# Kernel tuning notes

Hardware: AMD Instinct MI355X
Metric: run time of the kernel (lower is better)

The kernel has to match this reference:

```python
import jax, jax.numpy as jnp
import numpy as np

DECAY = 0.99
BETA = 0.25
EPS_NORM = 1e-12  # matches F.normalize eps


def _l2_normalize(x):
    n = jnp.linalg.norm(x, axis=-1, keepdims=True)
    return x / jnp.maximum(n, EPS_NORM)


def setup_inputs() -> dict:
    key = jax.random.key(0)
    ks = jax.random.split(key, 8)
    B, C, H, W = 16, 256, 64, 64
    D, K = 16, 4096  # codebook_dim, n_embed
    z = jax.random.normal(ks[0], (B, C, H, W), dtype=jnp.float32)
    # 1x1 convs == per-pixel linear layers
    w_down = jax.random.normal(ks[1], (D, C), dtype=jnp.float32) / np.sqrt(C).astype(np.float32)
    b_down = jnp.zeros((D,), dtype=jnp.float32)
    w_up = jax.random.normal(ks[2], (C, D), dtype=jnp.float32) / np.sqrt(D).astype(np.float32)
    b_up = jnp.zeros((C,), dtype=jnp.float32)
    embedding = jax.random.uniform(ks[3], (K, D), minval=-1.0 / K, maxval=1.0 / K, dtype=jnp.float32)
    cluster_size = jax.random.uniform(ks[4], (K,), minval=0.5, maxval=2.0, dtype=jnp.float32)
    embed_avg = jax.random.normal(ks[5], (K, D), dtype=jnp.float32) * 0.01
    return {"z": z, "w_down": w_down, "b_down": b_down, "w_up": w_up,
            "b_up": b_up, "embedding": embedding,
            "cluster_size": cluster_size, "embed_avg": embed_avg}


def reference(z, w_down, b_down, w_up, b_up, embedding, cluster_size, embed_avg):
    B, C, H, W = z.shape
    K, D = embedding.shape

    # proj_down: 1x1 conv -> per-token linear
    z_low = jnp.einsum('bchw,dc->bdhw', z, w_down) + b_down[None, :, None, None]
    z_flat = z_low.transpose(0, 2, 3, 1).reshape(-1, D)          # [N, D]
    z_norm = _l2_normalize(z_flat)
    e_norm = _l2_normalize(embedding)                             # [K, D]

    # squared L2 distances (argmin identical to cdist argmin)
    d2 = (jnp.sum(z_norm * z_norm, -1, keepdims=True)
          - 2.0 * z_norm @ e_norm.T
          + jnp.sum(e_norm * e_norm, -1)[None, :])               # [N, K]
    indices = jnp.argmin(d2, axis=-1)                             # [N]
    z_q_flat = e_norm[indices]                                    # [N, D]

    # EMA buffer update (training path); scatter-accumulate via segment_sum
    ones = jnp.ones(indices.shape, dtype=jnp.float32)
    batch_cluster_size = jax.ops.segment_sum(ones, indices, num_segments=K)
    batch_embed_sum = jax.ops.segment_sum(z_norm, indices, num_segments=K)
    new_cluster_size = cluster_size * DECAY + (1.0 - DECAY) * batch_cluster_size
    new_embed_avg = embed_avg * DECAY + (1.0 - DECAY) * batch_embed_sum
    n = new_cluster_size.sum()
    cs = (new_cluster_size + 1e-5) / (n + K * 1e-5) * n
    new_embedding = new_embed_avg / cs[:, None]

    commitment_loss = BETA * jnp.mean((z_norm - jax.lax.stop_gradient(z_q_flat)) ** 2)

    # straight-through estimator
    z_q_low_flat = z_norm + jax.lax.stop_gradient(z_q_flat - z_norm)
    z_q_low = z_q_low_flat.reshape(B, H, W, D).transpose(0, 3, 1, 2)
    z_q = jnp.einsum('bdhw,cd->bchw', z_q_low, w_up) + b_up[None, :, None, None]

    indices_2d = indices.reshape(B, H, W)

    # metrics / entropy loss (usage == bincount(indices))
    usage_prob = batch_cluster_size / (batch_cluster_size.sum() + 1e-8)
    entropy = -jnp.sum(usage_prob * jnp.log(usage_prob + 1e-8))
    entropy_loss = jnp.log(jnp.float32(K)) - entropy

    return (z_q, commitment_loss, indices_2d, entropy_loss,
            new_embedding, new_cluster_size, new_embed_avg)
```

## Files before the change

kernel.cpp:

```cpp
#include <hip/hip_runtime.h>
#include <math.h>

#define NTOK 65536
#define CDIM 256
#define DDIM 16
#define KCOD 4096
#define HWSZ 4096

#define DELTA 0.04f
#define KSPLIT2 8
#define KTPS (KCOD / 32 / KSPLIT2)

typedef short short8 __attribute__((ext_vector_type(8)));
typedef float f32x16 __attribute__((ext_vector_type(16)));

#define WS_ENORM 0
#define WS_ENN   (WS_ENORM + KCOD*DDIM)
#define WS_WDT   (WS_ENN + KCOD)
#define WS_EBF   (WS_WDT + CDIM*DDIM)
#define WS_ZN    (WS_EBF + KCOD*8)
#define WS_ZNBF  (WS_ZN + NTOK*DDIM)
#define WS_M1    (WS_ZNBF + NTOK*8)
#define WS_BCS   (WS_M1 + NTOK)
#define WS_BES   (WS_BCS + KCOD)
#define WS_SCAL  (WS_BES + KCOD*DDIM)
#define WS_PACK  (WS_SCAL + 8)

#define OFS_ZQ   0
#define OFS_LOSS 16777216
#define OFS_IDX  16777217
#define OFS_ENT  16842753
#define OFS_NE   16842754
#define OFS_NCS  16908290
#define OFS_NEA  16912386

__device__ inline unsigned f2bf2(float lo, float hi) {
  unsigned a = __float_as_uint(lo), b = __float_as_uint(hi);
  a = (a + 0x7FFFu + ((a >> 16) & 1u)) >> 16;
  b = (b + 0x7FFFu + ((b >> 16) & 1u)) >> 16;
  return a | (b << 16);
}
__device__ inline unsigned flipf(float f) {
  unsigned u = __float_as_uint(f);
  return (u & 0x80000000u) ? ~u : (u | 0x80000000u);
}
__device__ inline float unflipf(unsigned k) {
  unsigned u = (k & 0x80000000u) ? (k ^ 0x80000000u) : ~k;
  return __uint_as_float(u);
}

__global__ __launch_bounds__(256) void knorm_kernel(const float* __restrict__ emb,
                                                    const float* __restrict__ w_down,
                                                    float* __restrict__ ws) {
  int k = blockIdx.x * 256 + threadIdx.x;
  const float4* src = (const float4*)emb + (size_t)k * 4;
  float4 t0 = src[0], t1 = src[1], t2 = src[2], t3 = src[3];
  float e[16] = {t0.x,t0.y,t0.z,t0.w, t1.x,t1.y,t1.z,t1.w,
                 t2.x,t2.y,t2.z,t2.w, t3.x,t3.y,t3.z,t3.w};
  float ss = 0.f;
  #pragma unroll
  for (int d = 0; d < 16; ++d) ss += e[d] * e[d];
  float dn = fmaxf(sqrtf(ss), 1e-12f);
  #pragma unroll
  for (int d = 0; d < 16; ++d) e[d] = e[d] / dn;
  float s2 = 0.f;
  #pragma unroll
  for (int d = 0; d < 16; ++d) s2 += e[d] * e[d];
  float4* dst = (float4*)(ws + WS_ENORM) + (size_t)k * 4;
  dst[0] = make_float4(e[0],e[1],e[2],e[3]);
  dst[1] = make_float4(e[4],e[5],e[6],e[7]);
  dst[2] = make_float4(e[8],e[9],e[10],e[11]);
  dst[3] = make_float4(e[12],e[13],e[14],e[15]);
  ws[WS_ENN + k] = s2;
  ws[WS_WDT + k] = w_down[(k & 15) * 256 + (k >> 4)];
  uint4 p0 = make_uint4(f2bf2(e[0],e[1]),  f2bf2(e[2],e[3]),
                        f2bf2(e[4],e[5]),  f2bf2(e[6],e[7]));
  uint4 p1 = make_uint4(f2bf2(e[8],e[9]),  f2bf2(e[10],e[11]),
                        f2bf2(e[12],e[13]),f2bf2(e[14],e[15]));
  uint4* eb = (uint4*)(ws + WS_EBF) + (size_t)k * 2;
  eb[0] = p0; eb[1] = p1;
}

__global__ __launch_bounds__(256) void kdown_kernel(const float* __restrict__ z,
                                                    const float* __restrict__ wdt,
                                                    const float* __restrict__ b_down,
                                                    float* __restrict__ znp,
                                                    unsigned* __restrict__ znbf) {
  const int tid = threadIdx.x;
  const int n = blockIdx.x * 256 + tid;
  const int b = n >> 12;
  const int hw = n & 4095;
  const float* zp = z + (size_t)b * (CDIM * HWSZ) + hw;

  float acc[16];
  #pragma unroll
  for (int d = 0; d < 16; ++d) acc[d] = 0.f;

  #pragma unroll 16
  for (int c = 0; c < CDIM; ++c) {
    float zv = zp[(size_t)c * HWSZ];
    const float4* wr = (const float4*)(wdt + c * 16);
    float4 w0 = wr[0], w1 = wr[1], w2 = wr[2], w3 = wr[3];
    acc[0]  = fmaf(zv, w0.x, acc[0]);  acc[1]  = fmaf(zv, w0.y, acc[1]);
    acc[2]  = fmaf(zv, w0.z, acc[2]);  acc[3]  = fmaf(zv, w0.w, acc[3]);
    acc[4]  = fmaf(zv, w1.x, acc[4]);  acc[5]  = fmaf(zv, w1.y, acc[5]);
    acc[6]  = fmaf(zv, w1.z, acc[6]);  acc[7]  = fmaf(zv, w1.w, acc[7]);
    acc[8]  = fmaf(zv, w2.x, acc[8]);  acc[9]  = fmaf(zv, w2.y, acc[9]);
    acc[10] = fmaf(zv, w2.z, acc[10]); acc[11] = fmaf(zv, w2.w, acc[11]);
    acc[12] = fmaf(zv, w3.x, acc[12]); acc[13] = fmaf(zv, w3.y, acc[13]);
    acc[14] = fmaf(zv, w3.z, acc[14]); acc[15] = fmaf(zv, w3.w, acc[15]);
  }

  #pragma unroll
  for (int d = 0; d < 16; ++d) acc[d] = acc[d] + b_down[d];
  float ss = 0.f;
  #pragma unroll
  for (int d = 0; d < 16; ++d) ss += acc[d] * acc[d];
  float dn = fmaxf(sqrtf(ss), 1e-12f);
  #pragma unroll
  for (int d = 0; d < 16; ++d) acc[d] = acc[d] / dn;

  float4* op = (float4*)znp + (size_t)n * 4;
  op[0] = make_float4(acc[0],acc[1],acc[2],acc[3]);
  op[1] = make_float4(acc[4],acc[5],acc[6],acc[7]);
  op[2] = make_float4(acc[8],acc[9],acc[10],acc[11]);
  op[3] = make_float4(acc[12],acc[13],acc[14],acc[15]);

  uint4 p0 = make_uint4(f2bf2(acc[0],acc[1]),  f2bf2(acc[2],acc[3]),
                        f2bf2(acc[4],acc[5]),  f2bf2(acc[6],acc[7]));
  uint4 p1 = make_uint4(f2bf2(acc[8],acc[9]),  f2bf2(acc[10],acc[11]),
                        f2bf2(acc[12],acc[13]),f2bf2(acc[14],acc[15]));
  uint4* zb = (uint4*)znbf + (size_t)n * 2;
  zb[0] = p0; zb[1] = p1;
}

__global__ __launch_bounds__(256) void kmin_kernel(const unsigned* __restrict__ znbf,
                                                   const unsigned* __restrict__ ebf,
                                                   unsigned* __restrict__ m1u) {
  const int lane = threadIdx.x & 63;
  const int wv = threadIdx.x >> 6;
  const int tokbase = (blockIdx.x * 4 + wv) * 32;
  const int kt0 = blockIdx.y * KTPS;
  const int hi = lane >> 5;
  const int ln = lane & 31;

  const short8* za = (const short8*)znbf;
  const short8* eb = (const short8*)ebf;
  short8 afrag = za[(size_t)(tokbase + ln) * 2 + hi];

  float m[16];
  #pragma unroll
  for (int r = 0; r < 16; ++r) m[r] = -3.4e38f;

  #pragma unroll 4
  for (int kt = 0; kt < KTPS; ++kt) {
    short8 bfrag = eb[(size_t)((kt0 + kt) * 32 + ln) * 2 + hi];
    f32x16 acc;
    #pragma unroll
    for (int r = 0; r < 16; ++r) acc[r] = 0.f;
    acc = __builtin_amdgcn_mfma_f32_32x32x16_bf16(afrag, bfrag, acc, 0, 0, 0);
    #pragma unroll
    for (int r = 0; r < 16; ++r) m[r] = fmaxf(m[r], acc[r]);
  }

  #pragma unroll
  for (int r = 0; r < 16; ++r) {
    float v = m[r];
    v = fmaxf(v, __shfl_xor(v, 16, 32));
    v = fmaxf(v, __shfl_xor(v, 8, 32));
    v = fmaxf(v, __shfl_xor(v, 4, 32));
    v = fmaxf(v, __shfl_xor(v, 2, 32));
    v = fmaxf(v, __shfl_xor(v, 1, 32));
    m[r] = v;
  }
  if (ln == 0) {
    #pragma unroll
    for (int r = 0; r < 16; ++r) {
      int row = (r & 3) + 8 * (r >> 2) + 4 * hi;
      atomicMax(m1u + tokbase + row, flipf(m[r]));
    }
  }
}

__global__ __launch_bounds__(256) void kcand_kernel(const unsigned* __restrict__ znbf,
                                                    const unsigned* __restrict__ ebf,
                                                    const unsigned* __restrict__ m1u,
                                                    const float* __restrict__ enorm,
                                                    const float* __restrict__ ennp,
                                                    const float* __restrict__ znp,
                                                    unsigned long long* __restrict__ packp) {
  const int lane = threadIdx.x & 63;
  const int wv = threadIdx.x >> 6;
  const int tokbase = (blockIdx.x * 4 + wv) * 32;
  const int kt0 = blockIdx.y * KTPS;
  const int hi = lane >> 5;
  const int ln = lane & 31;

  const short8* za = (const short8*)znbf;
  const short8* eb = (const short8*)ebf;
  short8 afrag = za[(size_t)(tokbase + ln) * 2 + hi];

  float thr[16];
  #pragma unroll
  for (int r = 0; r < 16; ++r) {
    int row = (r & 3) + 8 * (r >> 2) + 4 * hi;
    thr[r] = unflipf(m1u[tokbase + row]) - DELTA;
  }

  for (int kt = 0; kt < KTPS; ++kt) {
    short8 bfrag = eb[(size_t)((kt0 + kt) * 32 + ln) * 2 + hi];
    f32x16 acc;
    #pragma unroll
    for (int r = 0; r < 16; ++r) acc[r] = 0.f;
    acc = __builtin_amdgcn_mfma_f32_32x32x16_bf16(afrag, bfrag, acc, 0, 0, 0);

    unsigned flags = 0u;
    #pragma unroll
    for (int r = 0; r < 16; ++r) flags |= (acc[r] >= thr[r]) ? (1u << r) : 0u;

    if (flags) {
      #pragma unroll
      for (int r = 0; r < 16; ++r) {
        if (flags & (1u << r)) {
          int row = (r & 3) + 8 * (r >> 2) + 4 * hi;
          int token = tokbase + row;
          int code = (kt0 + kt) * 32 + ln;
          const float4* znr4 = (const float4*)znp + (size_t)token * 4;
          const float4* er4  = (const float4*)enorm + (size_t)code * 4;
          float4 za0 = znr4[0], za1 = znr4[1], za2 = znr4[2], za3 = znr4[3];
          float4 eb0 = er4[0],  eb1 = er4[1],  eb2 = er4[2],  eb3 = er4[3];
          float dsc = ennp[code];
          dsc = fmaf(-2.f * za0.x, eb0.x, dsc); dsc = fmaf(-2.f * za0.y, eb0.y, dsc);
          dsc = fmaf(-2.f * za0.z, eb0.z, dsc); dsc = fmaf(-2.f * za0.w, eb0.w, dsc);
          dsc = fmaf(-2.f * za1.x, eb1.x, dsc); dsc = fmaf(-2.f * za1.y, eb1.y, dsc);
          dsc = fmaf(-2.f * za1.z, eb1.z, dsc); dsc = fmaf(-2.f * za1.w, eb1.w, dsc);
          dsc = fmaf(-2.f * za2.x, eb2.x, dsc); dsc = fmaf(-2.f * za2.y, eb2.y, dsc);
          dsc = fmaf(-2.f * za2.z, eb2.z, dsc); dsc = fmaf(-2.f * za2.w, eb2.w, dsc);
          dsc = fmaf(-2.f * za3.x, eb3.x, dsc); dsc = fmaf(-2.f * za3.y, eb3.y, dsc);
          dsc = fmaf(-2.f * za3.z, eb3.z, dsc); dsc = fmaf(-2.f * za3.w, eb3.w, dsc);
          unsigned u = __float_as_uint(dsc);
          u = (u & 0x80000000u) ? ~u : (u | 0x80000000u);
          unsigned long long key =
              ((unsigned long long)u << 32) | (unsigned)code;
          atomicMin(packp + token, key);
        }
      }
    }
  }
}

__global__ __launch_bounds__(256) void kfinal_kernel(const float* __restrict__ w_up,
                                                     const float* __restrict__ b_up,
                                                     const float* __restrict__ enorm,
                                                     const float* __restrict__ znp,
                                                     const unsigned long long* __restrict__ packp,
                                                     float* __restrict__ wsacc,
                                                     float* __restrict__ out) {
  const int tid = threadIdx.x;
  const int n = blockIdx.x * 256 + tid;
  const int bidx = (int)(unsigned)(packp[n] & 0xFFFFFFFFull);

  float zn[16];
  {
    const float4* zp = (const float4*)znp + (size_t)n * 4;
    float4 a0 = zp[0], a1 = zp[1], a2 = zp[2], a3 = zp[3];
    zn[0]=a0.x; zn[1]=a0.y; zn[2]=a0.z; zn[3]=a0.w;
    zn[4]=a1.x; zn[5]=a1.y; zn[6]=a1.z; zn[7]=a1.w;
    zn[8]=a2.x; zn[9]=a2.y; zn[10]=a2.z; zn[11]=a2.w;
    zn[12]=a3.x; zn[13]=a3.y; zn[14]=a3.z; zn[15]=a3.w;
  }
  float zq[16];
  {
    const float4* ebp = (const float4*)enorm + (size_t)bidx * 4;
    float4 q0 = ebp[0], q1 = ebp[1], q2 = ebp[2], q3 = ebp[3];
    zq[0]=q0.x; zq[1]=q0.y; zq[2]=q0.z; zq[3]=q0.w;
    zq[4]=q1.x; zq[5]=q1.y; zq[6]=q1.z; zq[7]=q1.w;
    zq[8]=q2.x; zq[9]=q2.y; zq[10]=q2.z; zq[11]=q2.w;
    zq[12]=q3.x; zq[13]=q3.y; zq[14]=q3.z; zq[15]=q3.w;
  }

  out[OFS_IDX + n] = (float)bidx;

  float ls = 0.f;
  #pragma unroll
  for (int d = 0; d < 16; ++d) { float df = zn[d] - zq[d]; ls = fmaf(df, df, ls); }

  atomicAdd(wsacc + bidx, 1.0f);
  #pragma unroll
  for (int d = 0; d < 16; ++d)
    atomicAdd(wsacc + KCOD + (size_t)bidx * 16 + d, zn[d]);

  #pragma unroll
  for (int off = 32; off > 0; off >>= 1) ls += __shfl_down(ls, off, 64);
  if ((tid & 63) == 0) atomicAdd(wsacc + KCOD + KCOD * DDIM + 0, ls);

  float ql[16];
  #pragma unroll
  for (int d = 0; d < 16; ++d) ql[d] = zn[d] + (zq[d] - zn[d]);

  const int b = n >> 12, hw = n & 4095;
  float* op = out + OFS_ZQ + (size_t)b * (CDIM * HWSZ) + hw;
  #pragma unroll 8
  for (int c = 0; c < CDIM; ++c) {
    const float4* wr = (const float4*)(w_up + c * 16);
    float4 w0 = wr[0], w1 = wr[1], w2 = wr[2], w3 = wr[3];
    float a = 0.f;
    a = fmaf(ql[0],  w0.x, a); a = fmaf(ql[1],  w0.y, a);
    a = fmaf(ql[2],  w0.z, a); a = fmaf(ql[3],  w0.w, a);
    a = fmaf(ql[4],  w1.x, a); a = fmaf(ql[5],  w1.y, a);
    a = fmaf(ql[6],  w1.z, a); a = fmaf(ql[7],  w1.w, a);
    a = fmaf(ql[8],  w2.x, a); a = fmaf(ql[9],  w2.y, a);
    a = fmaf(ql[10], w2.z, a); a = fmaf(ql[11], w2.w, a);
    a = fmaf(ql[12], w3.x, a); a = fmaf(ql[13], w3.y, a);
    a = fmaf(ql[14], w3.z, a); a = fmaf(ql[15], w3.w, a);
    a = a + b_up[c];
    op[(size_t)c * HWSZ] = a;
  }
}

__global__ __launch_bounds__(256) void kema_kernel(const float* __restrict__ cluster_size,
                                                   const float* __restrict__ embed_avg,
                                                   float* __restrict__ ws,
                                                   float* __restrict__ out) {
  const float DEC = 0.99f;
  const float OMD = (float)(1.0 - 0.99);
  const int k = blockIdx.x * 256 + threadIdx.x;
  float bcsv = ws[WS_BCS + k];
  float ncs = cluster_size[k] * DEC + OMD * bcsv;
  out[OFS_NCS + k] = ncs;
  #pragma unroll
  for (int d = 0; d < 16; ++d) {
    float nea = embed_avg[(size_t)k * 16 + d] * DEC + OMD * ws[WS_BES + (size_t)k * 16 + d];
    out[OFS_NEA + (size_t)k * 16 + d] = nea;
  }
  float p = bcsv / 65536.0f;
  float et = -p * logf(p + 1e-8f);

  __shared__ float r1[4], r2[4];
  float v1 = ncs, v2 = et;
  #pragma unroll
  for (int off = 32; off > 0; off >>= 1) {
    v1 += __shfl_down(v1, off, 64);
    v2 += __shfl_down(v2, off, 64);
  }
  int lane = threadIdx.x & 63, w = threadIdx.x >> 6;
  if (lane == 0) { r1[w] = v1; r2[w] = v2; }
  __syncthreads();
  if (threadIdx.x == 0) {
    atomicAdd(ws + WS_SCAL + 1, (r1[0] + r1[1]) + (r1[2] + r1[3]));
    atomicAdd(ws + WS_SCAL + 2, (r2[0] + r2[1]) + (r2[2] + r2[3]));
  }
}

__global__ __launch_bounds__(256) void kemb_kernel(const float* __restrict__ ws,
                                                   float* __restrict__ out) {
  const float KEPS = (float)(4096.0 * 1e-5);
  const int k = blockIdx.x * 256 + threadIdx.x;
  float n = ws[WS_SCAL + 1];
  float ncs = out[OFS_NCS + k];
  float cs = (ncs + 1e-5f) / (n + KEPS) * n;
  #pragma unroll
  for (int d = 0; d < 16; ++d)
    out[OFS_NE + (size_t)k * 16 + d] = out[OFS_NEA + (size_t)k * 16 + d] / cs;
  if (k == 0) {
    out[OFS_LOSS] = 0.25f * (ws[WS_SCAL + 0] / 1048576.0f);
    out[OFS_ENT]  = (float)8.317766166719343 - ws[WS_SCAL + 2];
  }
}

extern "C" void kernel_launch(void* const* d_in, const int* in_sizes, int n_in,
                              void* d_out, int out_size, void* d_ws, size_t ws_size,
                              hipStream_t stream) {
  const float* z        = (const float*)d_in[0];
  const float* w_down   = (const float*)d_in[1];
  const float* b_down   = (const float*)d_in[2];
  const float* w_up     = (const float*)d_in[3];
  const float* b_up     = (const float*)d_in[4];
  const float* emb      = (const float*)d_in[5];
  const float* csz      = (const float*)d_in[6];
  const float* eavg     = (const float*)d_in[7];
  float* out = (float*)d_out;
  float* ws  = (float*)d_ws;

  hipMemsetAsync(ws + WS_M1, 0,
                 (size_t)(NTOK + KCOD + KCOD*DDIM + 8) * sizeof(float), stream);
  hipMemsetAsync(ws + WS_PACK, 0xFF, (size_t)NTOK * 8, stream);

  knorm_kernel<<<KCOD / 256, 256, 0, stream>>>(emb, w_down, ws);
  kdown_kernel<<<NTOK / 256, 256, 0, stream>>>(z, ws + WS_WDT, b_down,
                                               ws + WS_ZN, (unsigned*)(ws + WS_ZNBF));
  kmin_kernel<<<dim3(NTOK / 128, KSPLIT2), 256, 0, stream>>>(
      (const unsigned*)(ws + WS_ZNBF), (const unsigned*)(ws + WS_EBF),
      (unsigned*)(ws + WS_M1));
  kcand_kernel<<<dim3(NTOK / 128, KSPLIT2), 256, 0, stream>>>(
      (const unsigned*)(ws + WS_ZNBF), (const unsigned*)(ws + WS_EBF),
      (const unsigned*)(ws + WS_M1), ws + WS_ENORM, ws + WS_ENN, ws + WS_ZN,
      (unsigned long long*)(ws + WS_PACK));
  kfinal_kernel<<<NTOK / 256, 256, 0, stream>>>(
      w_up, b_up, ws + WS_ENORM, ws + WS_ZN,
      (const unsigned long long*)(ws + WS_PACK), ws + WS_BCS, out);
  kema_kernel<<<KCOD / 256, 256, 0, stream>>>(csz, eavg, ws, out);
  kemb_kernel<<<KCOD / 256, 256, 0, stream>>>(ws, out);
}
```

Baseline: 275.0 us.

## Stage quantized vectors in LDS and write z_q output with float4 stores

The up-projection in the final kernel now stages each block's straight-through vectors in shared memory transposed by dimension. Each thread then computes 4 consecutive tokens for 64 of the 256 output channels, with each wave taking a quarter of the channels. Results are written with 128-bit float4 stores instead of scalar stores. The aim is wider, fully coalesced writes of the large z_q output and fewer weight loads per output element, at the cost of a block barrier, extra LDS use and more registers.

```diff
diff --git a/kernel.cpp b/kernel.cpp
--- a/kernel.cpp
+++ b/kernel.cpp
@@ -256,8 +256,11 @@
                                                      const unsigned long long* __restrict__ packp,
                                                      float* __restrict__ wsacc,
                                                      float* __restrict__ out) {
+  __shared__ float qlds[DDIM * 256];
   const int tid = threadIdx.x;
-  const int n = blockIdx.x * 256 + tid;
+  const int n0 = blockIdx.x * 256;
+  const int n = n0 + tid;
+
   const int bidx = (int)(unsigned)(packp[n] & 0xFFFFFFFFull);
 
   float zn[16];
@@ -294,27 +297,45 @@
   for (int off = 32; off > 0; off >>= 1) ls += __shfl_down(ls, off, 64);
   if ((tid & 63) == 0) atomicAdd(wsacc + KCOD + KCOD * DDIM + 0, ls);
 
-  float ql[16];
-  #pragma unroll
-  for (int d = 0; d < 16; ++d) ql[d] = zn[d] + (zq[d] - zn[d]);
-
-  const int b = n >> 12, hw = n & 4095;
-  float* op = out + OFS_ZQ + (size_t)b * (CDIM * HWSZ) + hw;
-  #pragma unroll 8
-  for (int c = 0; c < CDIM; ++c) {
+  #pragma unroll
+  for (int d = 0; d < 16; ++d) qlds[d * 256 + tid] = zn[d] + (zq[d] - zn[d]);
+  __syncthreads();
+
+  const int wv = tid >> 6;
+  const int q  = tid & 63;
+  const float4* qv = (const float4*)qlds;
+  float4 r[16];
+  #pragma unroll
+  for (int d = 0; d < 16; ++d) r[d] = qv[d * 64 + q];
+
+  const int b = n0 >> 12, hw0 = n0 & 4095;
+  float* opb = out + OFS_ZQ + (size_t)b * (CDIM * HWSZ) + hw0 + 4 * q;
+
+  #pragma unroll 4
+  for (int i = 0; i < 64; ++i) {
+    const int c = wv * 64 + i;
     const float4* wr = (const float4*)(w_up + c * 16);
     float4 w0 = wr[0], w1 = wr[1], w2 = wr[2], w3 = wr[3];
-    float a = 0.f;
-    a = fmaf(ql[0],  w0.x, a); a = fmaf(ql[1],  w0.y, a);
-    a = fmaf(ql[2],  w0.z, a); a = fmaf(ql[3],  w0.w, a);
-    a = fmaf(ql[4],  w1.x, a); a = fmaf(ql[5],  w1.y, a);
-    a = fmaf(ql[6],  w1.z, a); a = fmaf(ql[7],  w1.w, a);
-    a = fmaf(ql[8],  w2.x, a); a = fmaf(ql[9],  w2.y, a);
-    a = fmaf(ql[10], w2.z, a); a = fmaf(ql[11], w2.w, a);
-    a = fmaf(ql[12], w3.x, a); a = fmaf(ql[13], w3.y, a);
-    a = fmaf(ql[14], w3.z, a); a = fmaf(ql[15], w3.w, a);
-    a = a + b_up[c];
-    op[(size_t)c * HWSZ] = a;
+    float bu = b_up[c];
+    float a0 = 0.f, a1 = 0.f, a2 = 0.f, a3 = 0.f;
+    a0=fmaf(r[0].x,w0.x,a0); a1=fmaf(r[0].y,w0.x,a1); a2=fmaf(r[0].z,w0.x,a2); a3=fmaf(r[0].w,w0.x,a3);
+    a0=fmaf(r[1].x,w0.y,a0); a1=fmaf(r[1].y,w0.y,a1); a2=fmaf(r[1].z,w0.y,a2); a3=fmaf(r[1].w,w0.y,a3);
+    a0=fmaf(r[2].x,w0.z,a0); a1=fmaf(r[2].y,w0.z,a1); a2=fmaf(r[2].z,w0.z,a2); a3=fmaf(r[2].w,w0.z,a3);
+    a0=fmaf(r[3].x,w0.w,a0); a1=fmaf(r[3].y,w0.w,a1); a2=fmaf(r[3].z,w0.w,a2); a3=fmaf(r[3].w,w0.w,a3);
+    a0=fmaf(r[4].x,w1.x,a0); a1=fmaf(r[4].y,w1.x,a1); a2=fmaf(r[4].z,w1.x,a2); a3=fmaf(r[4].w,w1.x,a3);
+    a0=fmaf(r[5].x,w1.y,a0); a1=fmaf(r[5].y,w1.y,a1); a2=fmaf(r[5].z,w1.y,a2); a3=fmaf(r[5].w,w1.y,a3);
+    a0=fmaf(r[6].x,w1.z,a0); a1=fmaf(r[6].y,w1.z,a1); a2=fmaf(r[6].z,w1.z,a2); a3=fmaf(r[6].w,w1.z,a3);
+    a0=fmaf(r[7].x,w1.w,a0); a1=fmaf(r[7].y,w1.w,a1); a2=fmaf(r[7].z,w1.w,a2); a3=fmaf(r[7].w,w1.w,a3);
+    a0=fmaf(r[8].x,w2.x,a0); a1=fmaf(r[8].y,w2.x,a1); a2=fmaf(r[8].z,w2.x,a2); a3=fmaf(r[8].w,w2.x,a3);
+    a0=fmaf(r[9].x,w2.y,a0); a1=fmaf(r[9].y,w2.y,a1); a2=fmaf(r[9].z,w2.y,a2); a3=fmaf(r[9].w,w2.y,a3);
+    a0=fmaf(r[10].x,w2.z,a0); a1=fmaf(r[10].y,w2.z,a1); a2=fmaf(r[10].z,w2.z,a2); a3=fmaf(r[10].w,w2.z,a3);
+    a0=fmaf(r[11].x,w2.w,a0); a1=fmaf(r[11].y,w2.w,a1); a2=fmaf(r[11].z,w2.w,a2); a3=fmaf(r[11].w,w2.w,a3);
+    a0=fmaf(r[12].x,w3.x,a0); a1=fmaf(r[12].y,w3.x,a1); a2=fmaf(r[12].z,w3.x,a2); a3=fmaf(r[12].w,w3.x,a3);
+    a0=fmaf(r[13].x,w3.y,a0); a1=fmaf(r[13].y,w3.y,a1); a2=fmaf(r[13].z,w3.y,a2); a3=fmaf(r[13].w,w3.y,a3);
+    a0=fmaf(r[14].x,w3.z,a0); a1=fmaf(r[14].y,w3.z,a1); a2=fmaf(r[14].z,w3.z,a2); a3=fmaf(r[14].w,w3.z,a3);
+    a0=fmaf(r[15].x,w3.w,a0); a1=fmaf(r[15].y,w3.w,a1); a2=fmaf(r[15].z,w3.w,a2); a3=fmaf(r[15].w,w3.w,a3);
+    float4 st = make_float4(a0 + bu, a1 + bu, a2 + bu, a3 + bu);
+    *(float4*)(opb + (size_t)c * HWSZ) = st;
   }
 }
 
```

New measurement: 270.3 us. No clear change (-1.7%).

## Split final stage into merge and up-projection kernels with wider parallelism

Applied to the files above, without the earlier changes.

Splits the final per-token kernel into two. The first handles gather, loss and the scatter-add atomics with four threads per token, and writes the straight-through value back into workspace. The second does the up-projection with a 2D grid that divides output channels four ways, so each thread computes four tokens and issues float4 stores. The EMA and embedding kernels are also spread to one thread per element instead of one per code. This raises parallelism and store coalescing in the write-bound up-projection, at the cost of an extra launch and a workspace round trip for the quantized vectors.

```diff
diff --git a/kernel.cpp b/kernel.cpp
--- a/kernel.cpp
+++ b/kernel.cpp
@@ -10,6 +10,7 @@
 #define DELTA 0.04f
 #define KSPLIT2 8
 #define KTPS (KCOD / 32 / KSPLIT2)
+#define CSPLIT 4
 
 typedef short short8 __attribute__((ext_vector_type(8)));
 typedef float f32x16 __attribute__((ext_vector_type(16)));
@@ -249,72 +250,87 @@
   }
 }
 
-__global__ __launch_bounds__(256) void kfinal_kernel(const float* __restrict__ w_up,
-                                                     const float* __restrict__ b_up,
-                                                     const float* __restrict__ enorm,
-                                                     const float* __restrict__ znp,
+__global__ __launch_bounds__(256) void kmerge_kernel(const float* __restrict__ enorm,
+                                                     float* __restrict__ znql,
                                                      const unsigned long long* __restrict__ packp,
                                                      float* __restrict__ wsacc,
                                                      float* __restrict__ out) {
+  const int gid = blockIdx.x * 256 + threadIdx.x;
+  const int n = gid >> 2, qd = gid & 3;
+  const int bidx = (int)(unsigned)(packp[n] & 0xFFFFFFFFull);
+
+  float4* zp = (float4*)znql + (size_t)n * 4 + qd;
+  float4 znq = *zp;
+  float4 zqq = ((const float4*)enorm)[(size_t)bidx * 4 + qd];
+
+  float ls = 0.f;
+  {
+    float d0 = znq.x - zqq.x, d1 = znq.y - zqq.y;
+    float d2 = znq.z - zqq.z, d3 = znq.w - zqq.w;
+    ls = fmaf(d0, d0, ls); ls = fmaf(d1, d1, ls);
+    ls = fmaf(d2, d2, ls); ls = fmaf(d3, d3, ls);
+  }
+
+  float* bes = wsacc + KCOD + (size_t)bidx * 16 + qd * 4;
+  atomicAdd(bes + 0, znq.x); atomicAdd(bes + 1, znq.y);
+  atomicAdd(bes + 2, znq.z); atomicAdd(bes + 3, znq.w);
+  if (qd == 0) {
+    atomicAdd(wsacc + bidx, 1.0f);
+    out[OFS_IDX + n] = (float)bidx;
+  }
+
+  *zp = make_float4(znq.x + (zqq.x - znq.x), znq.y + (zqq.y - znq.y),
+                    znq.z + (zqq.z - znq.z), znq.w + (zqq.w - znq.w));
+
+  #pragma unroll
+  for (int off = 32; off > 0; off >>= 1) ls += __shfl_down(ls, off, 64);
+  if ((threadIdx.x & 63) == 0) atomicAdd(wsacc + KCOD + KCOD * DDIM + 0, ls);
+}
+
+__global__ __launch_bounds__(256) void kup_kernel(const float* __restrict__ w_up,
+                                                  const float* __restrict__ b_up,
+                                                  const float* __restrict__ ql,
+                                                  float* __restrict__ out) {
   const int tid = threadIdx.x;
-  const int n = blockIdx.x * 256 + tid;
-  const int bidx = (int)(unsigned)(packp[n] & 0xFFFFFFFFull);
-
-  float zn[16];
-  {
-    const float4* zp = (const float4*)znp + (size_t)n * 4;
-    float4 a0 = zp[0], a1 = zp[1], a2 = zp[2], a3 = zp[3];
-    zn[0]=a0.x; zn[1]=a0.y; zn[2]=a0.z; zn[3]=a0.w;
-    zn[4]=a1.x; zn[5]=a1.y; zn[6]=a1.z; zn[7]=a1.w;
-    zn[8]=a2.x; zn[9]=a2.y; zn[10]=a2.z; zn[11]=a2.w;
-    zn[12]=a3.x; zn[13]=a3.y; zn[14]=a3.z; zn[15]=a3.w;
-  }
-  float zq[16];
-  {
-    const float4* ebp = (const float4*)enorm + (size_t)bidx * 4;
-    float4 q0 = ebp[0], q1 = ebp[1], q2 = ebp[2], q3 = ebp[3];
-    zq[0]=q0.x; zq[1]=q0.y; zq[2]=q0.z; zq[3]=q0.w;
-    zq[4]=q1.x; zq[5]=q1.y; zq[6]=q1.z; zq[7]=q1.w;
-    zq[8]=q2.x; zq[9]=q2.y; zq[10]=q2.z; zq[11]=q2.w;
-    zq[12]=q3.x; zq[13]=q3.y; zq[14]=q3.z; zq[15]=q3.w;
-  }
-
-  out[OFS_IDX + n] = (float)bidx;
-
-  float ls = 0.f;
-  #pragma unroll
-  for (int d = 0; d < 16; ++d) { float df = zn[d] - zq[d]; ls = fmaf(df, df, ls); }
-
-  atomicAdd(wsacc + bidx, 1.0f);
-  #pragma unroll
-  for (int d = 0; d < 16; ++d)
-    atomicAdd(wsacc + KCOD + (size_t)bidx * 16 + d, zn[d]);
-
-  #pragma unroll
-  for (int off = 32; off > 0; off >>= 1) ls += __shfl_down(ls, off, 64);
-  if ((tid & 63) == 0) atomicAdd(wsacc + KCOD + KCOD * DDIM + 0, ls);
-
-  float ql[16];
-  #pragma unroll
-  for (int d = 0; d < 16; ++d) ql[d] = zn[d] + (zq[d] - zn[d]);
-
-  const int b = n >> 12, hw = n & 4095;
-  float* op = out + OFS_ZQ + (size_t)b * (CDIM * HWSZ) + hw;
-  #pragma unroll 8
-  for (int c = 0; c < CDIM; ++c) {
+  const int wv = tid >> 6, q = tid & 63;
+  const int n0 = blockIdx.x * 256;
+
+  const float4* qp = (const float4*)ql + ((size_t)n0 + 4 * q) * 4;
+  float4 t0[4], t1[4], t2[4], t3[4];
+  #pragma unroll
+  for (int j = 0; j < 4; ++j) {
+    t0[j] = qp[j]; t1[j] = qp[4 + j]; t2[j] = qp[8 + j]; t3[j] = qp[12 + j];
+  }
+
+  const int b = n0 >> 12, hw0 = n0 & 4095;
+  float* opb = out + OFS_ZQ + (size_t)b * (CDIM * HWSZ) + hw0 + 4 * q;
+  const int cbase = blockIdx.y * (CDIM / CSPLIT) + wv * 16;
+
+  #pragma unroll 4
+  for (int i = 0; i < 16; ++i) {
+    const int c = cbase + i;
     const float4* wr = (const float4*)(w_up + c * 16);
     float4 w0 = wr[0], w1 = wr[1], w2 = wr[2], w3 = wr[3];
-    float a = 0.f;
-    a = fmaf(ql[0],  w0.x, a); a = fmaf(ql[1],  w0.y, a);
-    a = fmaf(ql[2],  w0.z, a); a = fmaf(ql[3],  w0.w, a);
-    a = fmaf(ql[4],  w1.x, a); a = fmaf(ql[5],  w1.y, a);
-    a = fmaf(ql[6],  w1.z, a); a = fmaf(ql[7],  w1.w, a);
-    a = fmaf(ql[8],  w2.x, a); a = fmaf(ql[9],  w2.y, a);
-    a = fmaf(ql[10], w2.z, a); a = fmaf(ql[11], w2.w, a);
-    a = fmaf(ql[12], w3.x, a); a = fmaf(ql[13], w3.y, a);
-    a = fmaf(ql[14], w3.z, a); a = fmaf(ql[15], w3.w, a);
-    a = a + b_up[c];
-    op[(size_t)c * HWSZ] = a;
+    float bu = b_up[c];
+    float a0 = 0.f, a1 = 0.f, a2 = 0.f, a3 = 0.f;
+    a0=fmaf(t0[0].x,w0.x,a0); a1=fmaf(t1[0].x,w0.x,a1); a2=fmaf(t2[0].x,w0.x,a2); a3=fmaf(t3[0].x,w0.x,a3);
+    a0=fmaf(t0[0].y,w0.y,a0); a1=fmaf(t1[0].y,w0.y,a1); a2=fmaf(t2[0].y,w0.y,a2); a3=fmaf(t3[0].y,w0.y,a3);
+    a0=fmaf(t0[0].z,w0.z,a0); a1=fmaf(t1[0].z,w0.z,a1); a2=fmaf(t2[0].z,w0.z,a2); a3=fmaf(t3[0].z,w0.z,a3);
+    a0=fmaf(t0[0].w,w0.w,a0); a1=fmaf(t1[0].w,w0.w,a1); a2=fmaf(t2[0].w,w0.w,a2); a3=fmaf(t3[0].w,w0.w,a3);
+    a0=fmaf(t0[1].x,w1.x,a0); a1=fmaf(t1[1].x,w1.x,a1); a2=fmaf(t2[1].x,w1.x,a2); a3=fmaf(t3[1].x,w1.x,a3);
+    a0=fmaf(t0[1].y,w1.y,a0); a1=fmaf(t1[1].y,w1.y,a1); a2=fmaf(t2[1].y,w1.y,a2); a3=fmaf(t3[1].y,w1.y,a3);
+    a0=fmaf(t0[1].z,w1.z,a0); a1=fmaf(t1[1].z,w1.z,a1); a2=fmaf(t2[1].z,w1.z,a2); a3=fmaf(t3[1].z,w1.z,a3);
+    a0=fmaf(t0[1].w,w1.w,a0); a1=fmaf(t1[1].w,w1.w,a1); a2=fmaf(t2[1].w,w1.w,a2); a3=fmaf(t3[1].w,w1.w,a3);
+    a0=fmaf(t0[2].x,w2.x,a0); a1=fmaf(t1[2].x,w2.x,a1); a2=fmaf(t2[2].x,w2.x,a2); a3=fmaf(t3[2].x,w2.x,a3);
+    a0=fmaf(t0[2].y,w2.y,a0); a1=fmaf(t1[2].y,w2.y,a1); a2=fmaf(t2[2].y,w2.y,a2); a3=fmaf(t3[2].y,w2.y,a3);
+    a0=fmaf(t0[2].z,w2.z,a0); a1=fmaf(t1[2].z,w2.z,a1); a2=fmaf(t2[2].z,w2.z,a2); a3=fmaf(t3[2].z,w2.z,a3);
+    a0=fmaf(t0[2].w,w2.w,a0); a1=fmaf(t1[2].w,w2.w,a1); a2=fmaf(t2[2].w,w2.w,a2); a3=fmaf(t3[2].w,w2.w,a3);
+    a0=fmaf(t0[3].x,w3.x,a0); a1=fmaf(t1[3].x,w3.x,a1); a2=fmaf(t2[3].x,w3.x,a2); a3=fmaf(t3[3].x,w3.x,a3);
+    a0=fmaf(t0[3].y,w3.y,a0); a1=fmaf(t1[3].y,w3.y,a1); a2=fmaf(t2[3].y,w3.y,a2); a3=fmaf(t3[3].y,w3.y,a3);
+    a0=fmaf(t0[3].z,w3.z,a0); a1=fmaf(t1[3].z,w3.z,a1); a2=fmaf(t2[3].z,w3.z,a2); a3=fmaf(t3[3].z,w3.z,a3);
+    a0=fmaf(t0[3].w,w3.w,a0); a1=fmaf(t1[3].w,w3.w,a1); a2=fmaf(t2[3].w,w3.w,a2); a3=fmaf(t3[3].w,w3.w,a3);
+    *(float4*)(opb + (size_t)c * HWSZ) =
+        make_float4(a0 + bu, a1 + bu, a2 + bu, a3 + bu);
   }
 }
 
@@ -324,45 +340,41 @@
                                                    float* __restrict__ out) {
   const float DEC = 0.99f;
   const float OMD = (float)(1.0 - 0.99);
-  const int k = blockIdx.x * 256 + threadIdx.x;
-  float bcsv = ws[WS_BCS + k];
-  float ncs = cluster_size[k] * DEC + OMD * bcsv;
-  out[OFS_NCS + k] = ncs;
-  #pragma unroll
-  for (int d = 0; d < 16; ++d) {
-    float nea = embed_avg[(size_t)k * 16 + d] * DEC + OMD * ws[WS_BES + (size_t)k * 16 + d];
-    out[OFS_NEA + (size_t)k * 16 + d] = nea;
-  }
-  float p = bcsv / 65536.0f;
-  float et = -p * logf(p + 1e-8f);
-
-  __shared__ float r1[4], r2[4];
-  float v1 = ncs, v2 = et;
+  const int gid = blockIdx.x * 256 + threadIdx.x;
+  const int k = gid >> 4, d = gid & 15;
+  float nea = embed_avg[gid] * DEC + OMD * ws[WS_BES + gid];
+  out[OFS_NEA + gid] = nea;
+
+  float v1 = 0.f, v2 = 0.f;
+  if (d == 0) {
+    float bcsv = ws[WS_BCS + k];
+    float ncs = cluster_size[k] * DEC + OMD * bcsv;
+    out[OFS_NCS + k] = ncs;
+    float p = bcsv / 65536.0f;
+    v1 = ncs;
+    v2 = -p * logf(p + 1e-8f);
+  }
   #pragma unroll
   for (int off = 32; off > 0; off >>= 1) {
     v1 += __shfl_down(v1, off, 64);
     v2 += __shfl_down(v2, off, 64);
   }
-  int lane = threadIdx.x & 63, w = threadIdx.x >> 6;
-  if (lane == 0) { r1[w] = v1; r2[w] = v2; }
-  __syncthreads();
-  if (threadIdx.x == 0) {
-    atomicAdd(ws + WS_SCAL + 1, (r1[0] + r1[1]) + (r1[2] + r1[3]));
-    atomicAdd(ws + WS_SCAL + 2, (r2[0] + r2[1]) + (r2[2] + r2[3]));
+  if ((threadIdx.x & 63) == 0) {
+    atomicAdd(ws + WS_SCAL + 1, v1);
+    atomicAdd(ws + WS_SCAL + 2, v2);
   }
 }
 
 __global__ __launch_bounds__(256) void kemb_kernel(const float* __restrict__ ws,
                                                    float* __restrict__ out) {
   const float KEPS = (float)(4096.0 * 1e-5);
-  const int k = blockIdx.x * 256 + threadIdx.x;
+  const int gid = blockIdx.x * 256 + threadIdx.x;
+  const int k = gid >> 4;
   float n = ws[WS_SCAL + 1];
   float ncs = out[OFS_NCS + k];
   float cs = (ncs + 1e-5f) / (n + KEPS) * n;
-  #pragma unroll
-  for (int d = 0; d < 16; ++d)
-    out[OFS_NE + (size_t)k * 16 + d] = out[OFS_NEA + (size_t)k * 16 + d] / cs;
-  if (k == 0) {
+  out[OFS_NE + gid] = out[OFS_NEA + gid] / cs;
+  if (gid == 0) {
     out[OFS_LOSS] = 0.25f * (ws[WS_SCAL + 0] / 1048576.0f);
     out[OFS_ENT]  = (float)8.317766166719343 - ws[WS_SCAL + 2];
   }
@@ -396,9 +408,11 @@
       (const unsigned*)(ws + WS_ZNBF), (const unsigned*)(ws + WS_EBF),
       (const unsigned*)(ws + WS_M1), ws + WS_ENORM, ws + WS_ENN, ws + WS_ZN,
       (unsigned long long*)(ws + WS_PACK));
-  kfinal_kernel<<<NTOK / 256, 256, 0, stream>>>(
-      w_up, b_up, ws + WS_ENORM, ws + WS_ZN,
+  kmerge_kernel<<<NTOK * 4 / 256, 256, 0, stream>>>(
+      ws + WS_ENORM, ws + WS_ZN,
       (const unsigned long long*)(ws + WS_PACK), ws + WS_BCS, out);
-  kema_kernel<<<KCOD / 256, 256, 0, stream>>>(csz, eavg, ws, out);
-  kemb_kernel<<<KCOD / 256, 256, 0, stream>>>(ws, out);
-}
+  kup_kernel<<<dim3(NTOK / 256, CSPLIT), 256, 0, stream>>>(
+      w_up, b_up, ws + WS_ZN, out);
+  kema_kernel<<<KCOD * DDIM / 256, 256, 0, stream>>>(csz, eavg, ws, out);
+  kemb_kernel<<<KCOD * DDIM / 256, 256, 0, stream>>>(ws, out);
+}
```

Result: slower. 290.3 us (+5.6%).
